# Performance work log

Hardware: AMD Instinct MI355X
Metric: run time of the kernel (lower is better)

The kernel has to match this reference:

```python
import jax, jax.numpy as jnp
import numpy as np

D_MODEL = 1024
EXPAND = 4
D_INNER = EXPAND * D_MODEL  # 4096
D_STATE = 16
D_CONV = 4
DT_RANK = (D_MODEL + 15) // 16  # 64
B_SZ, L_SEQ = 2, 2048
EPS = 1e-5


def _quantize(w):
    # round(clamp(w / mean|w|, -1, 1)) -> ternary weights
    s = w / (jnp.mean(jnp.abs(w)) + 1e-8)
    return jnp.round(jnp.clip(s, -1.0, 1.0))


def setup_inputs() -> dict:
    key = jax.random.key(0)
    ks = jax.random.split(key, 16)
    f32 = jnp.float32
    x = jax.random.normal(ks[0], (B_SZ, L_SEQ, D_MODEL), dtype=f32)
    # LayerNorms
    g1 = jnp.ones((D_MODEL,), f32); b1 = jnp.zeros((D_MODEL,), f32)
    g2 = jnp.ones((D_MODEL,), f32); b2 = jnp.zeros((D_MODEL,), f32)
    # SwiGLU MLP (ternary-quantized weights, as in __init__)
    w1 = _quantize(jax.random.normal(ks[1], (EXPAND * D_MODEL, D_MODEL), f32) * 0.02)
    bias1 = jnp.zeros((EXPAND * D_MODEL,), f32)
    w2 = _quantize(jax.random.normal(ks[2], (D_MODEL, EXPAND * D_MODEL), f32) * 0.02)
    bias2 = jnp.zeros((D_MODEL,), f32)
    # Mamba params
    in_proj_w = jax.random.normal(ks[3], (2 * D_INNER, D_MODEL), f32) * 0.02
    conv_w = jax.random.normal(ks[4], (D_INNER, D_CONV), f32) * 0.2
    conv_b = jnp.zeros((D_INNER,), f32)
    x_proj_w = jax.random.normal(ks[5], (DT_RANK + 2 * D_STATE, D_INNER), f32) * 0.02
    dt_proj_w = jax.random.normal(ks[6], (D_INNER, DT_RANK), f32) * (DT_RANK ** -0.5)
    dt_proj_b = jnp.log(jnp.expm1(jnp.clip(
        jnp.exp(jax.random.uniform(ks[7], (D_INNER,), f32) * (np.log(0.1) - np.log(1e-3)) + np.log(1e-3)),
        1e-4, None)))  # standard mamba dt bias init
    A_log = jnp.log(jnp.broadcast_to(jnp.arange(1, D_STATE + 1, dtype=f32), (D_INNER, D_STATE)))
    D = jnp.ones((D_INNER,), f32)
    out_proj_w = jax.random.normal(ks[8], (D_MODEL, D_INNER), f32) * 0.02
    return dict(x=x, g1=g1, b1=b1, g2=g2, b2=b2, w1=w1, bias1=bias1, w2=w2, bias2=bias2,
                in_proj_w=in_proj_w, conv_w=conv_w, conv_b=conv_b, x_proj_w=x_proj_w,
                dt_proj_w=dt_proj_w, dt_proj_b=dt_proj_b, A_log=A_log, D=D,
                out_proj_w=out_proj_w)


def _layernorm(x, g, b):
    mu = jnp.mean(x, -1, keepdims=True)
    var = jnp.mean(jnp.square(x - mu), -1, keepdims=True)
    return (x - mu) * jax.lax.rsqrt(var + EPS) * g + b


def _mamba(xn, in_proj_w, conv_w, conv_b, x_proj_w, dt_proj_w, dt_proj_b, A_log, D, out_proj_w):
    B, L, _ = xn.shape
    xz = jnp.einsum('bld,ed->ble', xn, in_proj_w)  # [B,L,2*d_inner]
    u, z = jnp.split(xz, 2, axis=-1)
    # causal depthwise conv1d, kernel size D_CONV
    up = jnp.pad(u, ((0, 0), (D_CONV - 1, 0), (0, 0)))
    conv = conv_b + sum(up[:, k:k + L, :] * conv_w[:, k] for k in range(D_CONV))
    u = jax.nn.silu(conv)  # [B,L,d_inner]
    x_dbl = jnp.einsum('bld,ed->ble', u, x_proj_w)
    dt_in, Bm, Cm = jnp.split(x_dbl, [DT_RANK, DT_RANK + D_STATE], axis=-1)
    dt = jax.nn.softplus(jnp.einsum('blr,dr->bld', dt_in, dt_proj_w) + dt_proj_b)
    A = -jnp.exp(A_log)  # [d_inner, d_state]

    def step(h, inp):
        dt_t, B_t, C_t, u_t = inp  # [B,d_inner],[B,d_state],[B,d_state],[B,d_inner]
        dA = jnp.exp(dt_t[..., None] * A)              # [B,d_inner,d_state]
        h = dA * h + (dt_t * u_t)[..., None] * B_t[:, None, :]
        y = jnp.einsum('bds,bs->bd', h, C_t)
        return h, y

    h0 = jnp.zeros((B, D_INNER, D_STATE), xn.dtype)
    xs = (dt.swapaxes(0, 1), Bm.swapaxes(0, 1), Cm.swapaxes(0, 1), u.swapaxes(0, 1))
    _, ys = jax.lax.scan(step, h0, xs)
    y = ys.swapaxes(0, 1) + u * D
    y = y * jax.nn.silu(z)
    return jnp.einsum('ble,de->bld', y, out_proj_w)


def reference(x, g1, b1, g2, b2, w1, bias1, w2, bias2, in_proj_w, conv_w, conv_b,
              x_proj_w, dt_proj_w, dt_proj_b, A_log, D, out_proj_w):
    h = _layernorm(x, g1, b1)
    h = jax.nn.silu(jnp.einsum('bld,ed->ble', h, w1) + bias1)
    x = x + jnp.einsum('ble,de->bld', h, w2) + bias2
    x = x + _mamba(_layernorm(x, g2, b2), in_proj_w, conv_w, conv_b, x_proj_w,
                   dt_proj_w, dt_proj_b, A_log, D, out_proj_w)
    return x
```

## Files before the change

### kernel.cpp

```cpp
#include <hip/hip_runtime.h>
#include <cstdint>
#include <cstddef>


namespace {
constexpr int D_MODEL = 1024;
constexpr int D_INNER = 4096;
constexpr int D_STATE = 16;
constexpr int DT_RANK = 64;
constexpr int B_SZ    = 2;
constexpr int L_SEQ   = 2048;
constexpr int M_ROWS  = B_SZ * L_SEQ;
constexpr int LC      = 32;
constexpr int NCHUNK  = L_SEQ / LC;
}

typedef __bf16 bf16x8_t __attribute__((ext_vector_type(8)));
typedef float  f32x4    __attribute__((ext_vector_type(4)));
typedef unsigned short us8 __attribute__((ext_vector_type(8)));

__device__ __forceinline__ unsigned short f2bf(float f) {
  union { float f; unsigned int u; } v; v.f = f;
  unsigned int r = (v.u + 0x7fffu + ((v.u >> 16) & 1u)) >> 16;
  return (unsigned short)r;
}
__device__ __forceinline__ float bf2f(unsigned short s) {
  union { unsigned int u; float f; } v; v.u = ((unsigned int)s) << 16;
  return v.f;
}

__device__ __forceinline__ float softplus_fast(float v) {
  const float e = __builtin_amdgcn_exp2f(-fabsf(v) * 1.44269504088896f);
  return fmaxf(v, 0.f) + 0.693147180559945f * __builtin_amdgcn_logf(1.f + e);
}

__device__ __forceinline__ void gload16(const void* g, void* l) {
  __builtin_amdgcn_global_load_lds(
      (const __attribute__((address_space(1))) unsigned int*)g,
      (__attribute__((address_space(3))) unsigned int*)l, 16, 0, 0);
}

__global__ __launch_bounds__(256)
void cvt6(const float* __restrict__ s0, unsigned short* __restrict__ d0,
          const float* __restrict__ s1, unsigned short* __restrict__ d1,
          const float* __restrict__ s2, unsigned short* __restrict__ d2,
          const float* __restrict__ s3, unsigned short* __restrict__ d3,
          const float* __restrict__ s4, unsigned short* __restrict__ d4,
          const float* __restrict__ s5, unsigned short* __restrict__ d5) {
  int blk = blockIdx.x;
  const float* s; unsigned short* d;
  if (blk < 4096)                  { s = s0; d = d0; }
  else if ((blk -= 4096) < 4096)   { s = s1; d = d1; }
  else if ((blk -= 4096) < 8192)   { s = s2; d = d2; }
  else if ((blk -= 8192) < 384)    { s = s3; d = d3; }
  else if ((blk -= 384) < 256)     { s = s4; d = d4; }
  else { blk -= 256;                 s = s5; d = d5; }
  const int i = blk * 1024 + threadIdx.x * 4;
  float4 v = *(const float4*)(s + i);
  ushort4 o; o.x = f2bf(v.x); o.y = f2bf(v.y); o.z = f2bf(v.z); o.w = f2bf(v.w);
  *(ushort4*)(d + i) = o;
}

__global__ __launch_bounds__(256) void ln_bf16(const float* __restrict__ x,
                                               const float* __restrict__ g,
                                               const float* __restrict__ b,
                                               unsigned short* __restrict__ out) {
  const int row = blockIdx.x;
  const int tid = threadIdx.x;
  const float4 v = *(const float4*)(x + (size_t)row * D_MODEL + tid * 4);
  float s  = v.x + v.y + v.z + v.w;
  float s2 = v.x*v.x + v.y*v.y + v.z*v.z + v.w*v.w;
#pragma unroll
  for (int o = 32; o >= 1; o >>= 1) { s += __shfl_xor(s, o); s2 += __shfl_xor(s2, o); }
  __shared__ float red[8];
  if ((tid & 63) == 0) { red[(tid >> 6) * 2] = s; red[(tid >> 6) * 2 + 1] = s2; }
  __syncthreads();
  s  = red[0] + red[2] + red[4] + red[6];
  s2 = red[1] + red[3] + red[5] + red[7];
  const float mu  = s * (1.f / D_MODEL);
  const float var = s2 * (1.f / D_MODEL) - mu * mu;
  const float rstd = rsqrtf(var + 1e-5f);
  const float4 gv = *(const float4*)(g + tid * 4);
  const float4 bv = *(const float4*)(b + tid * 4);
  ushort4 o;
  o.x = f2bf((v.x - mu) * rstd * gv.x + bv.x);
  o.y = f2bf((v.y - mu) * rstd * gv.y + bv.y);
  o.z = f2bf((v.z - mu) * rstd * gv.z + bv.z);
  o.w = f2bf((v.w - mu) * rstd * gv.w + bv.w);
  *(ushort4*)(out + (size_t)row * D_MODEL + tid * 4) = o;
}

__global__ __launch_bounds__(256)
void combine_ln(const unsigned short* __restrict__ part, const float* __restrict__ bias,
                const float* __restrict__ res, const float* __restrict__ g,
                const float* __restrict__ b, float* __restrict__ x2out,
                unsigned short* __restrict__ xnout) {
  const int row = blockIdx.x;
  const int tid = threadIdx.x;
  const size_t i4 = (size_t)row * D_MODEL + tid * 4;
  constexpr size_t S = (size_t)M_ROWS * D_MODEL;
  float a0 = 0.f, a1 = 0.f, a2 = 0.f, a3 = 0.f;
#pragma unroll
  for (int z = 0; z < 4; ++z) {
    const ushort4 p = *(const ushort4*)(part + z * S + i4);
    a0 += bf2f(p.x); a1 += bf2f(p.y); a2 += bf2f(p.z); a3 += bf2f(p.w);
  }
  const float4 bv = *(const float4*)(bias + tid * 4);
  const float4 rv = *(const float4*)(res + i4);
  float4 v;
  v.x = a0 + bv.x + rv.x;
  v.y = a1 + bv.y + rv.y;
  v.z = a2 + bv.z + rv.z;
  v.w = a3 + bv.w + rv.w;
  *(float4*)(x2out + i4) = v;
  float s  = v.x + v.y + v.z + v.w;
  float s2 = v.x*v.x + v.y*v.y + v.z*v.z + v.w*v.w;
#pragma unroll
  for (int o = 32; o >= 1; o >>= 1) { s += __shfl_xor(s, o); s2 += __shfl_xor(s2, o); }
  __shared__ float red[8];
  if ((tid & 63) == 0) { red[(tid >> 6) * 2] = s; red[(tid >> 6) * 2 + 1] = s2; }
  __syncthreads();
  s  = red[0] + red[2] + red[4] + red[6];
  s2 = red[1] + red[3] + red[5] + red[7];
  const float mu  = s * (1.f / D_MODEL);
  const float var = s2 * (1.f / D_MODEL) - mu * mu;
  const float rstd = rsqrtf(var + 1e-5f);
  const float4 gv = *(const float4*)(g + tid * 4);
  const float4 b2 = *(const float4*)(b + tid * 4);
  ushort4 o;
  o.x = f2bf((v.x - mu) * rstd * gv.x + b2.x);
  o.y = f2bf((v.y - mu) * rstd * gv.y + b2.y);
  o.z = f2bf((v.z - mu) * rstd * gv.z + b2.z);
  o.w = f2bf((v.w - mu) * rstd * gv.w + b2.w);
  *(ushort4*)(xnout + i4) = o;
}

template<int EPI>
__global__ __launch_bounds__(512, 1)
void gemm256(const unsigned short* __restrict__ A, const unsigned short* __restrict__ W,
             int M, int N, int K, int lda, int ldw,
             const float* __restrict__ bias, void* __restrict__ out0) {
  if constexpr (EPI == 8) {
    const size_t koff = (size_t)blockIdx.z * K;
    A += koff; W += koff;
    out0 = (void*)((unsigned short*)out0 + (size_t)blockIdx.z * M * N);
  }
  __shared__ unsigned short smem[65536];
  const int tid  = threadIdx.x;
  const int w    = tid >> 6;
  const int lane = tid & 63;
  const int wr = w >> 2;
  const int wc = w & 3;
  const int fr = lane & 15;
  const int fq = lane >> 4;

  const int gx = gridDim.x, gy = gridDim.y;
  const int nwg = gx * gy;
  const int id  = blockIdx.y * gx + blockIdx.x;
  const int wid = (id & 7) * (nwg >> 3) + (id >> 3);
  const int n0 = (wid / gy) * 256;
  const int m0 = (wid % gy) * 256;

  const int srow  = tid >> 3;
  const int skelem = ((tid & 7) ^ (srow & 7)) * 8;

  int aslot[2];
#pragma unroll
  for (int ks = 0; ks < 2; ++ks) aslot[ks] = ((ks * 4 + fq) ^ (fr & 7)) * 8;

  f32x4 acc[8][4];
#pragma unroll
  for (int m = 0; m < 8; ++m)
#pragma unroll
    for (int n = 0; n < 4; ++n) acc[m][n] = f32x4{0.f, 0.f, 0.f, 0.f};

  const int NT = K >> 6;

  auto STAGE_HALF = [&](int half, int tn, unsigned short* Ad, unsigned short* Bd) {
    const int k0 = tn * 64;
    if (half < 2) {
#pragma unroll
      for (int li = 0; li < 2; ++li) {
        const int l = half * 2 + li;
        gload16(A + (size_t)(m0 + l * 64 + srow) * lda + k0 + skelem,
                Ad + (l * 64 + w * 8) * 64);
      }
    } else {
#pragma unroll
      for (int li = 0; li < 2; ++li) {
        const int l = (half - 2) * 2 + li;
        gload16(W + (size_t)(n0 + l * 64 + srow) * ldw + k0 + skelem,
                Bd + (l * 64 + w * 8) * 64);
      }
    }
  };

#pragma unroll
  for (int h = 0; h < 4; ++h) STAGE_HALF(h, 0, smem, smem + 32768);
  asm volatile("s_waitcnt vmcnt(0)" ::: "memory");
  __builtin_amdgcn_s_barrier();

  for (int t = 0; t < NT; ++t) {
    const int cur = t & 1;
    const unsigned short* Ab = smem + cur * 16384;
    const unsigned short* Bb = smem + 32768 + cur * 16384;
    unsigned short* Adn = smem + (cur ^ 1) * 16384;
    unsigned short* Bdn = smem + 32768 + (cur ^ 1) * 16384;
    const bool more = (t + 1 < NT);

    bf16x8_t af[4][2], bflo[2][2], bfhi[2][2];

#pragma unroll
    for (int mfi = 0; mfi < 4; ++mfi)
#pragma unroll
      for (int ks = 0; ks < 2; ++ks)
        af[mfi][ks] = *(const bf16x8_t*)
            &Ab[(wr * 128 + mfi * 16 + fr) * 64 + aslot[ks]];
#pragma unroll
    for (int nfi = 0; nfi < 2; ++nfi)
#pragma unroll
      for (int ks = 0; ks < 2; ++ks)
        bflo[nfi][ks] = *(const bf16x8_t*)
            &Bb[(wc * 64 + nfi * 16 + fr) * 64 + aslot[ks]];
    if (more) { STAGE_HALF(0, t + 1, Adn, Bdn); STAGE_HALF(1, t + 1, Adn, Bdn); }
    asm volatile("s_waitcnt lgkmcnt(0)" ::: "memory");
    __builtin_amdgcn_s_barrier();
    __builtin_amdgcn_s_setprio(1);
#pragma unroll
    for (int mfi = 0; mfi < 4; ++mfi)
#pragma unroll
      for (int nfi = 0; nfi < 2; ++nfi)
#pragma unroll
        for (int ks = 0; ks < 2; ++ks)
          acc[mfi][nfi] = __builtin_amdgcn_mfma_f32_16x16x32_bf16(
              af[mfi][ks], bflo[nfi][ks], acc[mfi][nfi], 0, 0, 0);
    __builtin_amdgcn_s_setprio(0);

#pragma unroll
    for (int nfi = 0; nfi < 2; ++nfi)
#pragma unroll
      for (int ks = 0; ks < 2; ++ks)
        bfhi[nfi][ks] = *(const bf16x8_t*)
            &Bb[(wc * 64 + (2 + nfi) * 16 + fr) * 64 + aslot[ks]];
    if (more) { STAGE_HALF(2, t + 1, Adn, Bdn); STAGE_HALF(3, t + 1, Adn, Bdn); }
    asm volatile("s_waitcnt lgkmcnt(0)" ::: "memory");
    __builtin_amdgcn_s_barrier();
    __builtin_amdgcn_s_setprio(1);
#pragma unroll
    for (int mfi = 0; mfi < 4; ++mfi)
#pragma unroll
      for (int nfi = 0; nfi < 2; ++nfi)
#pragma unroll
        for (int ks = 0; ks < 2; ++ks)
          acc[mfi][2 + nfi] = __builtin_amdgcn_mfma_f32_16x16x32_bf16(
              af[mfi][ks], bfhi[nfi][ks], acc[mfi][2 + nfi], 0, 0, 0);
    __builtin_amdgcn_s_setprio(0);

#pragma unroll
    for (int mfi = 0; mfi < 4; ++mfi)
#pragma unroll
      for (int ks = 0; ks < 2; ++ks)
        af[mfi][ks] = *(const bf16x8_t*)
            &Ab[(wr * 128 + (4 + mfi) * 16 + fr) * 64 + aslot[ks]];
    asm volatile("s_waitcnt lgkmcnt(0)" ::: "memory");
    __builtin_amdgcn_s_barrier();
    __builtin_amdgcn_s_setprio(1);
#pragma unroll
    for (int mfi = 0; mfi < 4; ++mfi)
#pragma unroll
      for (int nfi = 0; nfi < 2; ++nfi)
#pragma unroll
        for (int ks = 0; ks < 2; ++ks)
          acc[4 + mfi][nfi] = __builtin_amdgcn_mfma_f32_16x16x32_bf16(
              af[mfi][ks], bflo[nfi][ks], acc[4 + mfi][nfi], 0, 0, 0);
    __builtin_amdgcn_s_setprio(0);

    __builtin_amdgcn_s_setprio(1);
#pragma unroll
    for (int mfi = 0; mfi < 4; ++mfi)
#pragma unroll
      for (int nfi = 0; nfi < 2; ++nfi)
#pragma unroll
        for (int ks = 0; ks < 2; ++ks)
          acc[4 + mfi][2 + nfi] = __builtin_amdgcn_mfma_f32_16x16x32_bf16(
              af[mfi][ks], bfhi[nfi][ks], acc[4 + mfi][2 + nfi], 0, 0, 0);
    __builtin_amdgcn_s_setprio(0);

    asm volatile("s_waitcnt vmcnt(0)" ::: "memory");
    __builtin_amdgcn_s_barrier();
  }

  unsigned short* Cs = smem;
#pragma unroll
  for (int mf = 0; mf < 8; ++mf)
#pragma unroll
    for (int nf = 0; nf < 4; ++nf)
#pragma unroll
      for (int j = 0; j < 4; ++j) {
        const int row = wr * 128 + mf * 16 + fq * 4 + j;
        const int col = wc * 64 + nf * 16 + fr;
        float v = acc[mf][nf][j];
        if constexpr (EPI == 0) {
          v += bias[n0 + col];
          v = v / (1.f + __expf(-v));
        }
        Cs[row * 256 + ((((col >> 3) ^ (row & 7)) << 3) | (col & 7))] = f2bf(v);
      }
  __syncthreads();
  unsigned short* outp = (unsigned short*)out0;
  const int trow = tid >> 5;
  const int tg   = tid & 31;
#pragma unroll
  for (int i = 0; i < 16; ++i) {
    const int row = i * 16 + trow;
    const us8 vv = *(const us8*)&Cs[row * 256 + ((tg ^ (row & 7)) << 3)];
    unsigned short* dst = &outp[(size_t)(m0 + row) * N + n0 + tg * 8];
    if constexpr (EPI == 2) __builtin_nontemporal_store(vv, (us8*)dst);
    else                    *(us8*)dst = vv;
  }
}

template<int EPI>
__global__ __launch_bounds__(256)
void gemm_bt(const unsigned short* __restrict__ A, const unsigned short* __restrict__ W,
             int M, int N, int K, int lda, int ldw, int ldc,
             const float* __restrict__ bias, const float* __restrict__ res,
             void* __restrict__ out0) {
  if constexpr (EPI == 6) {
    const size_t koff = (size_t)blockIdx.z * K;
    A += koff; W += koff;
    out0 = (void*)((float*)out0 + (size_t)blockIdx.z * M * ldc);
  }
  const int gx = gridDim.x, gy = gridDim.y;
  const int nwg = gx * gy;
  const int id  = blockIdx.y * gx + blockIdx.x;
  const int wid = (nwg >= 8) ? ((id & 7) * (nwg >> 3) + (id >> 3)) : id;
  const int n0 = (wid / gy) * 128;
  const int m0 = (wid % gy) * 128;

  __shared__ unsigned short smem[16384];
  const int tid  = threadIdx.x;
  const int w    = tid >> 6;
  const int lane = tid & 63;
  const int wm = (w >> 1) * 64;
  const int wn = (w & 1) * 64;
  const int lrow = lane >> 2;
  const int lkb  = (lane & 3) * 8;
  const int fr   = lane & 15;
  const int fq   = lane >> 4;

  f32x4 acc[4][4];
#pragma unroll
  for (int m = 0; m < 4; ++m)
#pragma unroll
    for (int n = 0; n < 4; ++n) acc[m][n] = f32x4{0.f, 0.f, 0.f, 0.f};

  const int ar0 = m0 + (w * 2 + 0) * 16 + lrow;
  const int ar1 = m0 + (w * 2 + 1) * 16 + lrow;
  int br0 = n0 + (w * 2 + 0) * 16 + lrow; if (br0 > N - 1) br0 = N - 1;
  int br1 = n0 + (w * 2 + 1) * 16 + lrow; if (br1 > N - 1) br1 = N - 1;

  const int nk = K >> 5;
  auto STAGE = [&](int buf, int kt) {
    const int k0 = kt * 32;
    gload16(A + (size_t)ar0 * lda + k0 + lkb, smem + buf * 4096 + (w * 2 + 0) * 512);
    gload16(A + (size_t)ar1 * lda + k0 + lkb, smem + buf * 4096 + (w * 2 + 1) * 512);
    gload16(W + (size_t)br0 * ldw + k0 + lkb, smem + 8192 + buf * 4096 + (w * 2 + 0) * 512);
    gload16(W + (size_t)br1 * ldw + k0 + lkb, smem + 8192 + buf * 4096 + (w * 2 + 1) * 512);
  };
  STAGE(0, 0);
  if (nk > 1) STAGE(1, 1);

  for (int kt = 0; kt < nk; ++kt) {
    const int cur = kt & 1;
    if (kt + 1 < nk) asm volatile("s_waitcnt vmcnt(4)" ::: "memory");
    else             asm volatile("s_waitcnt vmcnt(0)" ::: "memory");
    __builtin_amdgcn_s_barrier();
    const unsigned short* Ac = smem + cur * 4096;
    const unsigned short* Bc = smem + 8192 + cur * 4096;
    bf16x8_t af[4], bf[4];
#pragma unroll
    for (int m = 0; m < 4; ++m) af[m] = *(const bf16x8_t*)&Ac[(wm + m * 16 + fr) * 32 + fq * 8];
#pragma unroll
    for (int n = 0; n < 4; ++n) bf[n] = *(const bf16x8_t*)&Bc[(wn + n * 16 + fr) * 32 + fq * 8];
    __builtin_amdgcn_s_setprio(1);
#pragma unroll
    for (int m = 0; m < 4; ++m)
#pragma unroll
      for (int n = 0; n < 4; ++n)
        acc[m][n] = __builtin_amdgcn_mfma_f32_16x16x32_bf16(af[m], bf[n], acc[m][n], 0, 0, 0);
    __builtin_amdgcn_s_setprio(0);
    asm volatile("s_waitcnt lgkmcnt(0)" ::: "memory");
    __builtin_amdgcn_s_barrier();
    if (kt + 2 < nk) STAGE(cur, kt + 2);
  }

  if constexpr (EPI == 6) {
#pragma unroll
    for (int m = 0; m < 4; ++m)
#pragma unroll
      for (int n = 0; n < 4; ++n)
#pragma unroll
        for (int j = 0; j < 4; ++j) {
          const int r = m0 + wm + m * 16 + fq * 4 + j;
          const int c = n0 + wn + n * 16 + fr;
          if (c >= N) continue;
          ((float*)out0)[(size_t)r * ldc + c] = acc[m][n][j];
        }
  } else {
    unsigned short* Cs = smem;
#pragma unroll
    for (int m = 0; m < 4; ++m)
#pragma unroll
      for (int n = 0; n < 4; ++n)
#pragma unroll
        for (int j = 0; j < 4; ++j) {
          const int row = wm + m * 16 + fq * 4 + j;
          const int col = wn + n * 16 + fr;
          float v = acc[m][n][j];
          if constexpr (EPI == 4) v = softplus_fast(v + bias[n0 + col]);
          Cs[row * 128 + ((((col >> 3) ^ (row & 7)) << 3) | (col & 7))] = f2bf(v);
        }
    __syncthreads();
    unsigned short* outp = (unsigned short*)out0;
    const int trow = tid >> 4;
    const int tg   = tid & 15;
#pragma unroll
    for (int i = 0; i < 8; ++i) {
      const int row = i * 16 + trow;
      const us8 vv = *(const us8*)&Cs[row * 128 + ((tg ^ (row & 7)) << 3)];
      *(us8*)&outp[(size_t)(m0 + row) * ldc + n0 + tg * 8] = vv;
    }
  }
}

__global__ __launch_bounds__(256)
void splitk_combine_bf(const unsigned short* __restrict__ part,
                       const float* __restrict__ res, float* __restrict__ out) {
  const size_t i4 = ((size_t)blockIdx.x * 256 + threadIdx.x) * 4;
  constexpr size_t S = (size_t)M_ROWS * D_MODEL;
  float a0 = 0.f, a1 = 0.f, a2 = 0.f, a3 = 0.f;
#pragma unroll
  for (int z = 0; z < 4; ++z) {
    const ushort4 p = *(const ushort4*)(part + z * S + i4);
    a0 += bf2f(p.x); a1 += bf2f(p.y); a2 += bf2f(p.z); a3 += bf2f(p.w);
  }
  const float4 r = *(const float4*)(res + i4);
  *(float4*)(out + i4) = float4{a0 + r.x, a1 + r.y, a2 + r.z, a3 + r.w};
}

__global__ __launch_bounds__(256)
void conv_silu_k(const unsigned short* __restrict__ xz, const float* __restrict__ cw,
                 const float* __restrict__ cb, unsigned short* __restrict__ uc) {
  const size_t idx = (size_t)blockIdx.x * 256 + threadIdx.x;
  const int dg  = (int)(idx & 511) * 8;
  const int row = (int)(idx >> 9);
  const int l   = row & (L_SEQ - 1);
  const unsigned short* up = xz + (size_t)row * (2 * D_INNER) + dg;
  us8 t0 = {0,0,0,0,0,0,0,0}, t1 = {0,0,0,0,0,0,0,0}, t2 = {0,0,0,0,0,0,0,0};
  const us8 t3 = *(const us8*)(up);
  if (l >= 1) t2 = *(const us8*)(up - (ptrdiff_t)1 * 2 * D_INNER);
  if (l >= 2) t1 = *(const us8*)(up - (ptrdiff_t)2 * 2 * D_INNER);
  if (l >= 3) t0 = *(const us8*)(up - (ptrdiff_t)3 * 2 * D_INNER);
  us8 o;
#pragma unroll
  for (int j = 0; j < 8; ++j) {
    const float4 w4 = *(const float4*)(cw + (dg + j) * 4);
    float acc = cb[dg + j];
    acc += bf2f(t0[j]) * w4.x;
    acc += bf2f(t1[j]) * w4.y;
    acc += bf2f(t2[j]) * w4.z;
    acc += bf2f(t3[j]) * w4.w;
    o[j] = f2bf(acc / (1.f + __expf(-acc)));
  }
  *(us8*)(uc + (size_t)row * D_INNER + dg) = o;
}

__global__ __launch_bounds__(256)
void xproj_combine(const float* __restrict__ part, unsigned short* __restrict__ dtin,
                   float* __restrict__ Bm, float* __restrict__ Cm) {
  const int idx = blockIdx.x * 256 + threadIdx.x;
  const int r = idx / 96, c = idx - r * 96;
  constexpr size_t S = (size_t)M_ROWS * 96;
  float v = 0.f;
#pragma unroll
  for (int z = 0; z < 8; ++z) v += part[idx + z * S];
  if (c < DT_RANK)            dtin[(size_t)r * DT_RANK + c] = f2bf(v);
  else if (c < DT_RANK + 16)  Bm[(size_t)r * 16 + (c - DT_RANK)] = v;
  else                        Cm[(size_t)r * 16 + (c - DT_RANK - 16)] = v;
}

__global__ __launch_bounds__(128)
void scan_part(const unsigned short* __restrict__ dt, const unsigned short* __restrict__ uc,
               const float* __restrict__ Bm, const float* __restrict__ A_log,
               float* __restrict__ Q, float* __restrict__ sumdt) {
  __shared__ float sB[LC][D_STATE];
  const int lt = threadIdx.x;
  const int d  = blockIdx.x * 128 + lt;
  const int c  = blockIdx.y;
  const int b  = blockIdx.z;
  const size_t rowbase = (size_t)b * L_SEQ + (size_t)c * LC;
  ((float4*)&sB[0][0])[lt] = ((const float4*)(Bm + rowbase * D_STATE))[lt];
  float Ap[D_STATE];
#pragma unroll
  for (int s = 0; s < D_STATE; ++s)
    Ap[s] = -__expf(A_log[d * D_STATE + s]) * 1.44269504088896f;
  float h[D_STATE];
#pragma unroll
  for (int s = 0; s < D_STATE; ++s) h[s] = 0.f;
  float sdt = 0.f;
  __syncthreads();
  for (int t = 0; t < LC; ++t) {
    const size_t row = rowbase + t;
    const float dtv = bf2f(dt[row * D_INNER + d]);
    const float uv  = bf2f(uc[row * D_INNER + d]);
    sdt += dtv;
    const float du = dtv * uv;
    const float4* bp = (const float4*)&sB[t][0];
    const float4 b0 = bp[0], b1 = bp[1], b2 = bp[2], b3 = bp[3];
    const float Bv[16] = {b0.x,b0.y,b0.z,b0.w, b1.x,b1.y,b1.z,b1.w,
                          b2.x,b2.y,b2.z,b2.w, b3.x,b3.y,b3.z,b3.w};
#pragma unroll
    for (int s = 0; s < D_STATE; ++s) {
      const float dA = __builtin_amdgcn_exp2f(dtv * Ap[s]);
      h[s] = fmaf(dA, h[s], du * Bv[s]);
    }
  }
  float* q = Q + ((((size_t)b * NCHUNK + c) * D_INNER + d) << 4);
#pragma unroll
  for (int s = 0; s < D_STATE; s += 4)
    *(float4*)(q + s) = float4{h[s], h[s+1], h[s+2], h[s+3]};
  sumdt[((size_t)b * NCHUNK + c) * D_INNER + d] = sdt;
}

__global__ __launch_bounds__(256)
void scan_carry(float* __restrict__ Q, const float* __restrict__ sumdt,
                const float* __restrict__ A_log) {
  const int idx = blockIdx.x * 256 + threadIdx.x;
  const int s = idx & 15;
  const int d = (idx >> 4) & (D_INNER - 1);
  const int b = idx >> 16;
  const float Ap = -__expf(A_log[d * D_STATE + s]) * 1.44269504088896f;
  float h = 0.f;
  for (int c = 0; c < NCHUNK; ++c) {
    const size_t base = ((size_t)b * NCHUNK + c) * D_INNER;
    const size_t qoff = ((base + d) << 4) + s;
    const float q = Q[qoff];
    const float P = __builtin_amdgcn_exp2f(sumdt[base + d] * Ap);
    Q[qoff] = h;
    h = fmaf(P, h, q);
  }
}

__global__ __launch_bounds__(128)
void scan_final(const unsigned short* __restrict__ dt, const unsigned short* __restrict__ uc,
                const float* __restrict__ Bm, const float* __restrict__ Cm,
                unsigned short* __restrict__ xz, const float* __restrict__ A_log,
                const float* __restrict__ Dvec, const float* __restrict__ Hin) {
  __shared__ float sB[LC][D_STATE];
  __shared__ float sC[LC][D_STATE];
  const int lt = threadIdx.x;
  const int d  = blockIdx.x * 128 + lt;
  const int c  = blockIdx.y;
  const int b  = blockIdx.z;
  const size_t rowbase = (size_t)b * L_SEQ + (size_t)c * LC;
  ((float4*)&sB[0][0])[lt] = ((const float4*)(Bm + rowbase * D_STATE))[lt];
  ((float4*)&sC[0][0])[lt] = ((const float4*)(Cm + rowbase * D_STATE))[lt];
  float Ap[D_STATE];
#pragma unroll
  for (int s = 0; s < D_STATE; ++s)
    Ap[s] = -__expf(A_log[d * D_STATE + s]) * 1.44269504088896f;
  float h[D_STATE];
  const float* hin = Hin + ((((size_t)b * NCHUNK + c) * D_INNER + d) << 4);
#pragma unroll
  for (int s = 0; s < D_STATE; s += 4) {
    const float4 hv = *(const float4*)(hin + s);
    h[s] = hv.x; h[s+1] = hv.y; h[s+2] = hv.z; h[s+3] = hv.w;
  }
  const float Dv = Dvec[d];
  __syncthreads();
  for (int t = 0; t < LC; ++t) {
    const size_t row = rowbase + t;
    const float dtv = bf2f(dt[row * D_INNER + d]);
    const float uv  = bf2f(uc[row * D_INNER + d]);
    const float zv  = bf2f(xz[row * (2 * D_INNER) + D_INNER + d]);
    const float du = dtv * uv;
    const float4* bp = (const float4*)&sB[t][0];
    const float4 b0 = bp[0], b1 = bp[1], b2 = bp[2], b3 = bp[3];
    const float Bv[16] = {b0.x,b0.y,b0.z,b0.w, b1.x,b1.y,b1.z,b1.w,
                          b2.x,b2.y,b2.z,b2.w, b3.x,b3.y,b3.z,b3.w};
    const float4* cp = (const float4*)&sC[t][0];
    const float4 c0 = cp[0], c1 = cp[1], c2 = cp[2], c3 = cp[3];
    const float Cv[16] = {c0.x,c0.y,c0.z,c0.w, c1.x,c1.y,c1.z,c1.w,
                          c2.x,c2.y,c2.z,c2.w, c3.x,c3.y,c3.z,c3.w};
    float y0 = 0.f, y1 = 0.f;
#pragma unroll
    for (int s = 0; s < D_STATE; s += 2) {
      const float dA0 = __builtin_amdgcn_exp2f(dtv * Ap[s]);
      const float dA1 = __builtin_amdgcn_exp2f(dtv * Ap[s+1]);
      h[s]   = fmaf(dA0, h[s],   du * Bv[s]);
      h[s+1] = fmaf(dA1, h[s+1], du * Bv[s+1]);
      y0 = fmaf(h[s],   Cv[s],   y0);
      y1 = fmaf(h[s+1], Cv[s+1], y1);
    }
    const float yo = (y0 + y1 + uv * Dv) * (zv / (1.f + __expf(-zv)));
    xz[row * (2 * D_INNER) + d] = f2bf(yo);
  }
}

extern "C" void kernel_launch(void* const* d_in, const int* in_sizes, int n_in,
                              void* d_out, int out_size, void* d_ws, size_t ws_size,
                              hipStream_t stream) {
  (void)in_sizes; (void)n_in; (void)out_size; (void)ws_size;
  const float* x     = (const float*)d_in[0];
  const float* g1    = (const float*)d_in[1];
  const float* b1    = (const float*)d_in[2];
  const float* g2    = (const float*)d_in[3];
  const float* b2    = (const float*)d_in[4];
  const float* w1    = (const float*)d_in[5];
  const float* bias1 = (const float*)d_in[6];
  const float* w2    = (const float*)d_in[7];
  const float* bias2 = (const float*)d_in[8];
  const float* ipw   = (const float*)d_in[9];
  const float* cw    = (const float*)d_in[10];
  const float* cb    = (const float*)d_in[11];
  const float* xpw   = (const float*)d_in[12];
  const float* dtw   = (const float*)d_in[13];
  const float* dtbv  = (const float*)d_in[14];
  const float* A_log = (const float*)d_in[15];
  const float* Dvec  = (const float*)d_in[16];
  const float* opw   = (const float*)d_in[17];

  char* ws = (char*)d_ws;
  size_t off = 0;
  auto alloc = [&](size_t bytes) { void* p = ws + off; off = (off + bytes + 255) & ~(size_t)255; return p; };

  unsigned short* w1b  = (unsigned short*)alloc((size_t)D_INNER * D_MODEL * 2);
  unsigned short* w2b  = (unsigned short*)alloc((size_t)D_MODEL * D_INNER * 2);
  unsigned short* ipb  = (unsigned short*)alloc((size_t)2 * D_INNER * D_MODEL * 2);
  unsigned short* xpb  = (unsigned short*)alloc((size_t)96 * D_INNER * 2);
  unsigned short* dtb  = (unsigned short*)alloc((size_t)D_INNER * DT_RANK * 2);
  unsigned short* opb  = (unsigned short*)alloc((size_t)D_MODEL * D_INNER * 2);
  unsigned short* xn   = (unsigned short*)alloc((size_t)M_ROWS * D_MODEL * 2);
  unsigned short* hid  = (unsigned short*)alloc((size_t)M_ROWS * D_INNER * 2);
  float*          x2   = (float*)alloc((size_t)M_ROWS * D_MODEL * 4);
  unsigned short* xz   = (unsigned short*)alloc((size_t)M_ROWS * 2 * D_INNER * 2);
  unsigned short* dtbf = (unsigned short*)alloc((size_t)M_ROWS * D_INNER * 2);
  unsigned short* dtin = (unsigned short*)alloc((size_t)M_ROWS * DT_RANK * 2);
  float*          Bmb  = (float*)alloc((size_t)M_ROWS * 16 * 4);
  float*          Cmb  = (float*)alloc((size_t)M_ROWS * 16 * 4);
  float*          xpart= (float*)alloc((size_t)8 * M_ROWS * 96 * 4);
  float*          Qbuf = (float*)alloc((size_t)B_SZ * NCHUNK * D_INNER * 16 * 4);
  unsigned short* ucb  = hid;
  float*          sumdt = xpart;
  unsigned short* pA   = (unsigned short*)xz;
  unsigned short* pB   = dtbf;

  cvt6<<<21120, 256, 0, stream>>>(w1, w1b, w2, w2b, ipw, ipb, xpw, xpb, dtw, dtb, opw, opb);

  ln_bf16<<<M_ROWS, 256, 0, stream>>>(x, g1, b1, xn);
  gemm256<0><<<dim3(D_INNER / 256, M_ROWS / 256), 512, 0, stream>>>(
      xn, w1b, M_ROWS, D_INNER, D_MODEL, D_MODEL, D_MODEL, bias1, hid);
  gemm256<8><<<dim3(D_MODEL / 256, M_ROWS / 256, 4), 512, 0, stream>>>(
      hid, w2b, M_ROWS, D_MODEL, D_INNER / 4, D_INNER, D_INNER, nullptr, pA);
  combine_ln<<<M_ROWS, 256, 0, stream>>>(pA, bias2, x, g2, b2, x2, xn);

  gemm256<2><<<dim3(2 * D_INNER / 256, M_ROWS / 256), 512, 0, stream>>>(
      xn, ipb, M_ROWS, 2 * D_INNER, D_MODEL, D_MODEL, D_MODEL, nullptr, xz);
  conv_silu_k<<<(size_t)M_ROWS * 512 / 256, 256, 0, stream>>>(xz, cw, cb, ucb);

  gemm_bt<6><<<dim3(1, M_ROWS / 128, 8), 256, 0, stream>>>(
      ucb, xpb, M_ROWS, 96, 512, D_INNER, D_INNER, 96,
      nullptr, nullptr, xpart);
  xproj_combine<<<M_ROWS * 96 / 256, 256, 0, stream>>>(xpart, dtin, Bmb, Cmb);

  gemm_bt<4><<<dim3(D_INNER / 128, M_ROWS / 128), 256, 0, stream>>>(
      dtin, dtb, M_ROWS, D_INNER, DT_RANK, DT_RANK, DT_RANK, D_INNER, dtbv, nullptr, dtbf);

  scan_part<<<dim3(D_INNER / 128, NCHUNK, B_SZ), 128, 0, stream>>>(
      dtbf, ucb, Bmb, A_log, Qbuf, sumdt);
  scan_carry<<<B_SZ * D_INNER * 16 / 256, 256, 0, stream>>>(Qbuf, sumdt, A_log);
  scan_final<<<dim3(D_INNER / 128, NCHUNK, B_SZ), 128, 0, stream>>>(
      dtbf, ucb, Bmb, Cmb, xz, A_log, Dvec, Qbuf);

  gemm256<8><<<dim3(D_MODEL / 256, M_ROWS / 256, 4), 512, 0, stream>>>(
      xz, opb, M_ROWS, D_MODEL, D_INNER / 4, 2 * D_INNER, D_INNER, nullptr, pB);
  splitk_combine_bf<<<M_ROWS * D_MODEL / 1024, 256, 0, stream>>>(pB, x2, (float*)d_out);
}
```

Baseline: 447.6 us.

## Fuse causal conv+SiLU into in_proj GEMM epilogue with tile-boundary fixup

Splits the in_proj GEMM into two launches. The x half runs the depthwise causal conv and SiLU directly on the tile held in shared memory and writes the conv output. The z half is stored as before. Because the first three rows of each 256-row tile need the previous tile's last rows, those edge rows are saved to a side buffer and recomputed by a small fixup kernel. This removes the separate conv kernel's reread of the x half of xz and its write, at the cost of an extra launch, a heavier epilogue and some boundary complexity.

```diff
diff --git a/kernel.cpp b/kernel.cpp
--- a/kernel.cpp
+++ b/kernel.cpp
@@ -138,12 +138,14 @@
 template<int EPI>
 __global__ __launch_bounds__(512, 1)
 void gemm256(const unsigned short* __restrict__ A, const unsigned short* __restrict__ W,
-             int M, int N, int K, int lda, int ldw,
-             const float* __restrict__ bias, void* __restrict__ out0) {
+             int M, int N, int K, int lda, int ldw, int ldc,
+             const float* __restrict__ bias, void* __restrict__ out0,
+             const float* __restrict__ cw, const float* __restrict__ cb,
+             unsigned short* __restrict__ uside) {
   if constexpr (EPI == 8) {
     const size_t koff = (size_t)blockIdx.z * K;
     A += koff; W += koff;
-    out0 = (void*)((unsigned short*)out0 + (size_t)blockIdx.z * M * N);
+    out0 = (void*)((unsigned short*)out0 + (size_t)blockIdx.z * M * ldc);
   }
   __shared__ unsigned short smem[65536];
   const int tid  = threadIdx.x;
@@ -310,13 +312,75 @@
   unsigned short* outp = (unsigned short*)out0;
   const int trow = tid >> 5;
   const int tg   = tid & 31;
+  auto ldrow = [&](int r) -> us8 {
+    const int rr = r < 0 ? 0 : r;
+    return *(const us8*)&Cs[rr * 256 + ((tg ^ (rr & 7)) << 3)];
+  };
 #pragma unroll
   for (int i = 0; i < 16; ++i) {
     const int row = i * 16 + trow;
-    const us8 vv = *(const us8*)&Cs[row * 256 + ((tg ^ (row & 7)) << 3)];
-    unsigned short* dst = &outp[(size_t)(m0 + row) * N + n0 + tg * 8];
-    if constexpr (EPI == 2) __builtin_nontemporal_store(vv, (us8*)dst);
-    else                    *(us8*)dst = vv;
+    const us8 vv = ldrow(row);
+    if constexpr (EPI == 3) {
+      if (row < 3 || row >= 253) {
+        const int sel = row < 3 ? row : row - 250;
+        *(us8*)&uside[(((size_t)(m0 >> 8) * 6 + sel) * 4096) + n0 + tg * 8] = vv;
+      }
+      const us8 vm1 = ldrow(row - 1);
+      const us8 vm2 = ldrow(row - 2);
+      const us8 vm3 = ldrow(row - 3);
+      us8 o;
+#pragma unroll
+      for (int j = 0; j < 8; ++j) {
+        const int ch = n0 + tg * 8 + j;
+        const float4 w4 = *(const float4*)(cw + ch * 4);
+        float a = cb[ch];
+        a += bf2f(vm3[j]) * w4.x + bf2f(vm2[j]) * w4.y +
+             bf2f(vm1[j]) * w4.z + bf2f(vv[j]) * w4.w;
+        o[j] = f2bf(a / (1.f + __expf(-a)));
+      }
+      *(us8*)&outp[(size_t)(m0 + row) * ldc + n0 + tg * 8] = o;
+    } else {
+      unsigned short* dst = &outp[(size_t)(m0 + row) * ldc + n0 + tg * 8];
+      if constexpr (EPI == 2) __builtin_nontemporal_store(vv, (us8*)dst);
+      else                    *(us8*)dst = vv;
+    }
+  }
+}
+
+__global__ __launch_bounds__(256)
+void conv_fixup(const unsigned short* __restrict__ uside, const float* __restrict__ cw,
+                const float* __restrict__ cb, unsigned short* __restrict__ uc) {
+  const int idx = blockIdx.x * 256 + threadIdx.x;
+  const int tm = idx >> 9;
+  const int g8 = (idx & 511) * 8;
+  const int m0 = tm << 8;
+  auto sideld = [&](int t, int sel) -> us8 {
+    return *(const us8*)&uside[(((size_t)t * 6 + sel) * 4096) + g8];
+  };
+  const us8 zero = {0, 0, 0, 0, 0, 0, 0, 0};
+  us8 cur[3];
+  cur[0] = sideld(tm, 0); cur[1] = sideld(tm, 1); cur[2] = sideld(tm, 2);
+  us8 p3 = zero, p4 = zero, p5 = zero;
+  const bool seqstart = ((m0 & (L_SEQ - 1)) == 0);
+  if (!seqstart) { p3 = sideld(tm - 1, 3); p4 = sideld(tm - 1, 4); p5 = sideld(tm - 1, 5); }
+#pragma unroll
+  for (int r = 0; r < 3; ++r) {
+    const int l = (m0 & (L_SEQ - 1)) + r;
+    const us8 t3v = cur[r];
+    const us8 t2v = (l >= 1) ? (r >= 1 ? cur[r - 1] : p5) : zero;
+    const us8 t1v = (l >= 2) ? (r >= 2 ? cur[0] : (r == 1 ? p5 : p4)) : zero;
+    const us8 t0v = (l >= 3) ? (r == 2 ? p5 : (r == 1 ? p4 : p3)) : zero;
+    us8 o;
+#pragma unroll
+    for (int j = 0; j < 8; ++j) {
+      const int ch = g8 + j;
+      const float4 w4 = *(const float4*)(cw + ch * 4);
+      float a = cb[ch];
+      a += bf2f(t0v[j]) * w4.x + bf2f(t1v[j]) * w4.y +
+           bf2f(t2v[j]) * w4.z + bf2f(t3v[j]) * w4.w;
+      o[j] = f2bf(a / (1.f + __expf(-a)));
+    }
+    *(us8*)&uc[(size_t)(m0 + r) * D_INNER + g8] = o;
   }
 }
 
@@ -447,33 +511,6 @@
   }
   const float4 r = *(const float4*)(res + i4);
   *(float4*)(out + i4) = float4{a0 + r.x, a1 + r.y, a2 + r.z, a3 + r.w};
-}
-
-__global__ __launch_bounds__(256)
-void conv_silu_k(const unsigned short* __restrict__ xz, const float* __restrict__ cw,
-                 const float* __restrict__ cb, unsigned short* __restrict__ uc) {
-  const size_t idx = (size_t)blockIdx.x * 256 + threadIdx.x;
-  const int dg  = (int)(idx & 511) * 8;
-  const int row = (int)(idx >> 9);
-  const int l   = row & (L_SEQ - 1);
-  const unsigned short* up = xz + (size_t)row * (2 * D_INNER) + dg;
-  us8 t0 = {0,0,0,0,0,0,0,0}, t1 = {0,0,0,0,0,0,0,0}, t2 = {0,0,0,0,0,0,0,0};
-  const us8 t3 = *(const us8*)(up);
-  if (l >= 1) t2 = *(const us8*)(up - (ptrdiff_t)1 * 2 * D_INNER);
-  if (l >= 2) t1 = *(const us8*)(up - (ptrdiff_t)2 * 2 * D_INNER);
-  if (l >= 3) t0 = *(const us8*)(up - (ptrdiff_t)3 * 2 * D_INNER);
-  us8 o;
-#pragma unroll
-  for (int j = 0; j < 8; ++j) {
-    const float4 w4 = *(const float4*)(cw + (dg + j) * 4);
-    float acc = cb[dg + j];
-    acc += bf2f(t0[j]) * w4.x;
-    acc += bf2f(t1[j]) * w4.y;
-    acc += bf2f(t2[j]) * w4.z;
-    acc += bf2f(t3[j]) * w4.w;
-    o[j] = f2bf(acc / (1.f + __expf(-acc)));
-  }
-  *(us8*)(uc + (size_t)row * D_INNER + dg) = o;
 }
 
 __global__ __launch_bounds__(256)
@@ -651,6 +688,7 @@
   float*          Cmb  = (float*)alloc((size_t)M_ROWS * 16 * 4);
   float*          xpart= (float*)alloc((size_t)8 * M_ROWS * 96 * 4);
   float*          Qbuf = (float*)alloc((size_t)B_SZ * NCHUNK * D_INNER * 16 * 4);
+  unsigned short* uside= (unsigned short*)alloc((size_t)16 * 6 * D_INNER * 2);
   unsigned short* ucb  = hid;
   float*          sumdt = xpart;
   unsigned short* pA   = (unsigned short*)xz;
@@ -660,14 +698,20 @@
 
   ln_bf16<<<M_ROWS, 256, 0, stream>>>(x, g1, b1, xn);
   gemm256<0><<<dim3(D_INNER / 256, M_ROWS / 256), 512, 0, stream>>>(
-      xn, w1b, M_ROWS, D_INNER, D_MODEL, D_MODEL, D_MODEL, bias1, hid);
+      xn, w1b, M_ROWS, D_INNER, D_MODEL, D_MODEL, D_MODEL, D_INNER, bias1, hid,
+      nullptr, nullptr, nullptr);
   gemm256<8><<<dim3(D_MODEL / 256, M_ROWS / 256, 4), 512, 0, stream>>>(
-      hid, w2b, M_ROWS, D_MODEL, D_INNER / 4, D_INNER, D_INNER, nullptr, pA);
+      hid, w2b, M_ROWS, D_MODEL, D_INNER / 4, D_INNER, D_INNER, D_MODEL, nullptr, pA,
+      nullptr, nullptr, nullptr);
   combine_ln<<<M_ROWS, 256, 0, stream>>>(pA, bias2, x, g2, b2, x2, xn);
 
-  gemm256<2><<<dim3(2 * D_INNER / 256, M_ROWS / 256), 512, 0, stream>>>(
-      xn, ipb, M_ROWS, 2 * D_INNER, D_MODEL, D_MODEL, D_MODEL, nullptr, xz);
-  conv_silu_k<<<(size_t)M_ROWS * 512 / 256, 256, 0, stream>>>(xz, cw, cb, ucb);
+  gemm256<3><<<dim3(D_INNER / 256, M_ROWS / 256), 512, 0, stream>>>(
+      xn, ipb, M_ROWS, D_INNER, D_MODEL, D_MODEL, D_MODEL, D_INNER, nullptr, ucb,
+      cw, cb, uside);
+  gemm256<2><<<dim3(D_INNER / 256, M_ROWS / 256), 512, 0, stream>>>(
+      xn, ipb + (size_t)D_INNER * D_MODEL, M_ROWS, D_INNER, D_MODEL, D_MODEL, D_MODEL,
+      2 * D_INNER, nullptr, xz + D_INNER, nullptr, nullptr, nullptr);
+  conv_fixup<<<32, 256, 0, stream>>>(uside, cw, cb, ucb);
 
   gemm_bt<6><<<dim3(1, M_ROWS / 128, 8), 256, 0, stream>>>(
       ucb, xpb, M_ROWS, 96, 512, D_INNER, D_INNER, 96,
@@ -684,6 +728,7 @@
       dtbf, ucb, Bmb, Cmb, xz, A_log, Dvec, Qbuf);
 
   gemm256<8><<<dim3(D_MODEL / 256, M_ROWS / 256, 4), 512, 0, stream>>>(
-      xz, opb, M_ROWS, D_MODEL, D_INNER / 4, 2 * D_INNER, D_INNER, nullptr, pB);
+      xz, opb, M_ROWS, D_MODEL, D_INNER / 4, 2 * D_INNER, D_INNER, D_MODEL, nullptr, pB,
+      nullptr, nullptr, nullptr);
   splitk_combine_bf<<<M_ROWS * D_MODEL / 1024, 256, 0, stream>>>(pB, x2, (float*)d_out);
 }
```

Measured after the change: 568.0 us. 1.27x slower.
